# Optimization experiments

Measured on AMD Instinct MI355X. Metric: run time of the kernel, lower is better.

## Reference

```python
import jax, jax.numpy as jnp
import numpy as np

B, S = 4, 2048          # batch, seq tokens
D_IN, D_HID = 1280, 2048  # from CAMERAMOE emb_size / d_inner
E, K = 8, 2             # num_experts, top_k
LN_EPS = 1e-6


def setup_inputs() -> dict:
    key = jax.random.key(0)
    ks = jax.random.split(key, 8)
    rn = lambda k, shp, sc=1.0: jax.random.normal(k, shp, dtype=jnp.float32) * sc
    return {
        "x": rn(ks[0], (B, S, D_IN)),
        "noise": rn(ks[1], (B, S, E)),          # the randn_like draw, made explicit
        "wr": rn(ks[2], (D_IN, E), 0.02), "br": jnp.zeros((E,), jnp.float32),
        "wn": rn(ks[3], (D_IN, E), 0.02), "bn": jnp.zeros((E,), jnp.float32),
        "w1": rn(ks[4], (E, D_IN, D_HID), 0.02), "b1": jnp.zeros((E, D_HID), jnp.float32),
        "w2": rn(ks[5], (E, D_HID, D_IN), 0.02), "b2": jnp.zeros((E, D_IN), jnp.float32),
        "gamma": jnp.ones((E, D_IN), jnp.float32), "beta": jnp.zeros((E, D_IN), jnp.float32),
    }


def reference(x, noise, wr, br, wn, bn, w1, b1, w2, b2, gamma, beta):
    # --- NoisyTopkRouter ---
    logits = x @ wr + br                                  # [B,S,E]
    noise_logits = x @ wn + bn                            # [B,S,E]
    noisy = logits + noise * jax.nn.softplus(noise_logits)
    _, idx = jax.lax.top_k(noisy, K)                      # [B,S,K]
    sel = jax.nn.one_hot(idx, E, dtype=bool).any(axis=-2) # [B,S,E] selected-expert mask
    sparse_logits = jnp.where(sel, noisy, -jnp.inf)       # scatter of top-k logits into -inf
    gates = jax.nn.softmax(sparse_logits, axis=-1)        # zeros for non-selected experts

    # --- SparseMoE combine (gate-weighted sum over experts; gate==0 masks out
    # non-selected tokens, matching the torch masked gather/scatter-add math) ---
    h = jax.nn.relu(jnp.einsum('bsd,edh->ebsh', x, w1) + b1[:, None, None, :])
    y = jnp.einsum('ebsh,ehd->ebsd', h, w2) + b2[:, None, None, :]
    y = y + x                                             # residual (broadcast over E)
    mu = y.mean(axis=-1, keepdims=True)
    var = y.var(axis=-1, keepdims=True)
    y = (y - mu) * jax.lax.rsqrt(var + LN_EPS)
    y = y * gamma[:, None, None, :] + beta[:, None, None, :]
    return jnp.einsum('ebsd,bse->bsd', y, gates)          # [B,S,D_IN]
```

## Files before the change

### kernel.cpp

```cpp
#include <hip/hip_runtime.h>
#include <stdint.h>

typedef unsigned short u16;
typedef __attribute__((ext_vector_type(8))) short short8;
typedef __attribute__((ext_vector_type(4))) float f32x4;
typedef __attribute__((ext_vector_type(4))) float float4v;
typedef __attribute__((ext_vector_type(4))) unsigned short us4;
typedef __attribute__((ext_vector_type(8))) unsigned short us8;

#define TOK   8192
#define DIN   1280
#define DHID  2048
#define NEXP  8
#define RCAP  17408
#define MT128 136

#define TRBLK1 5120
#define TRBLK2 5120

__device__ __forceinline__ float bf2f(u16 u) {
  union { unsigned int i; float f; } v; v.i = ((unsigned int)u) << 16; return v.f;
}
__device__ __forceinline__ u16 f2bf(float f) {
  union { float f; unsigned int i; } v; v.f = f;
  unsigned int x = v.i;
  return (u16)((x + 0x7fffu + ((x >> 16) & 1u)) >> 16);
}

__device__ __forceinline__ void gload16(const u16* g, void* lds) {
  __builtin_amdgcn_global_load_lds(
      (const __attribute__((address_space(1))) unsigned int*)g,
      (__attribute__((address_space(3))) unsigned int*)lds, 16, 0, 0);
}

__global__ __launch_bounds__(256) void tr_k(
    const float* __restrict__ w1, u16* __restrict__ W1t,
    const float* __restrict__ w2, u16* __restrict__ W2t)
{
  __shared__ u16 ldsT[64 * 72];
  int id = blockIdx.x;
  int tid = threadIdx.x;
  int w = tid >> 6, lane = tid & 63;

  const float* in; u16* outp; int RK, CN, rb, cb;
  if (id < TRBLK1) {
    int e = id / 640, r = id % 640;
    RK = DIN; CN = DHID;
    rb = (r >> 5) * 64; cb = (r & 31) * 64;
    in = w1 + (size_t)e * RK * CN; outp = W1t + (size_t)e * RK * CN;
  } else {
    int id2 = id - TRBLK1;
    int e = id2 / 640, r = id2 % 640;
    RK = DHID; CN = DIN;
    rb = (r / 20) * 64; cb = (r % 20) * 64;
    in = w2 + (size_t)e * RK * CN; outp = W2t + (size_t)e * RK * CN;
  }
  {
    const float* src = in + (size_t)(rb + lane) * CN + cb + w * 16;
    u16 val[16];
    #pragma unroll
    for (int k = 0; k < 4; k++) {
      float4v v = *(const float4v*)(src + k * 4);
      #pragma unroll
      for (int j = 0; j < 4; j++) val[k * 4 + j] = f2bf(v[j]);
    }
    #pragma unroll
    for (int j = 0; j < 16; j++)
      ldsT[(w * 16 + j) * 72 + lane] = val[j];
  }
  __syncthreads();
  {
    int oc = tid >> 2, rch = (tid & 3) * 16;
    const u16* s = &ldsT[oc * 72 + rch];
    u16* d = outp + (size_t)(cb + oc) * RK + rb + rch;
    *(us8*)(d)     = *(const us8*)(s);
    *(us8*)(d + 8) = *(const us8*)(s + 8);
  }
}

__global__ __launch_bounds__(256) void router_k(
    const float* __restrict__ x, const float* __restrict__ noise,
    const float* __restrict__ wr, const float* __restrict__ br,
    const float* __restrict__ wn, const float* __restrict__ bn,
    int* __restrict__ topk_e, float* __restrict__ topk_g)
{
  int w = threadIdx.x >> 6, lane = threadIdx.x & 63;
  int t0 = blockIdx.x * 8 + w * 2;
  int h = lane & 1, dl = lane >> 1;
  const float* xA = x + (size_t)t0 * DIN;
  const float* xB = xA + DIN;

  float ra[4], na[4], rb2[4], nb2[4];
  #pragma unroll
  for (int j = 0; j < 4; j++) { ra[j] = 0.f; na[j] = 0.f; rb2[j] = 0.f; nb2[j] = 0.f; }

  #pragma unroll 4
  for (int d0 = 0; d0 < DIN; d0 += 32) {
    int d = d0 + dl;
    float4v wrv = *(const float4v*)(wr + (size_t)d * 8 + h * 4);
    float4v wnv = *(const float4v*)(wn + (size_t)d * 8 + h * 4);
    float xa = xA[d], xb = xB[d];
    #pragma unroll
    for (int j = 0; j < 4; j++) {
      ra[j]  += xa * wrv[j]; na[j]  += xa * wnv[j];
      rb2[j] += xb * wrv[j]; nb2[j] += xb * wnv[j];
    }
  }
  #pragma unroll
  for (int off = 2; off < 64; off <<= 1) {
    #pragma unroll
    for (int j = 0; j < 4; j++) {
      ra[j]  += __shfl_xor(ra[j],  off);
      na[j]  += __shfl_xor(na[j],  off);
      rb2[j] += __shfl_xor(rb2[j], off);
      nb2[j] += __shfl_xor(nb2[j], off);
    }
  }
  float raO[4], naO[4], rbO[4], nbO[4];
  #pragma unroll
  for (int j = 0; j < 4; j++) {
    raO[j] = __shfl_xor(ra[j], 1);
    naO[j] = __shfl_xor(na[j], 1);
    rbO[j] = __shfl_xor(rb2[j], 1);
    nbO[j] = __shfl_xor(nb2[j], 1);
  }
  if (lane == 0) {
    #pragma unroll
    for (int tt = 0; tt < 2; tt++) {
      int t = t0 + tt;
      float noisy[8];
      #pragma unroll
      for (int j = 0; j < 4; j++) {
        float lg0 = (tt ? rb2[j] : ra[j]) + br[j];
        float nl0 = (tt ? nb2[j] : na[j]) + bn[j];
        float lg1 = (tt ? rbO[j] : raO[j]) + br[4 + j];
        float nl1 = (tt ? nbO[j] : naO[j]) + bn[4 + j];
        float sp0 = (nl0 > 0.f) ? nl0 + log1pf(expf(-nl0)) : log1pf(expf(nl0));
        float sp1 = (nl1 > 0.f) ? nl1 + log1pf(expf(-nl1)) : log1pf(expf(nl1));
        noisy[j]     = lg0 + noise[(size_t)t * 8 + j] * sp0;
        noisy[4 + j] = lg1 + noise[(size_t)t * 8 + 4 + j] * sp1;
      }
      int e0 = 0; float v0 = noisy[0];
      #pragma unroll
      for (int e = 1; e < 8; e++) if (noisy[e] > v0) { v0 = noisy[e]; e0 = e; }
      int e1 = -1; float v1 = -1e30f;
      #pragma unroll
      for (int e = 0; e < 8; e++) if (e != e0 && noisy[e] > v1) { v1 = noisy[e]; e1 = e; }
      float g0 = 1.f / (1.f + expf(v1 - v0));
      topk_e[2*t] = e0; topk_e[2*t+1] = e1;
      topk_g[2*t] = g0; topk_g[2*t+1] = 1.f - g0;
    }
  }
}

__global__ __launch_bounds__(1024) void scan_k(
    const int* __restrict__ topk_e, int* __restrict__ rowmap, int* __restrict__ aoffs)
{
  __shared__ int cnt[1024][8];
  __shared__ int tot[8];
  __shared__ int base[8];
  int tid = threadIdx.x;
  int ebuf[16];
  #pragma unroll
  for (int j = 0; j < 16; j++) ebuf[j] = topk_e[tid * 16 + j];
  int c0=0,c1=0,c2=0,c3=0,c4=0,c5=0,c6=0,c7=0;
  #pragma unroll
  for (int j = 0; j < 16; j++) {
    int e = ebuf[j];
    c0 += (e==0); c1 += (e==1); c2 += (e==2); c3 += (e==3);
    c4 += (e==4); c5 += (e==5); c6 += (e==6); c7 += (e==7);
  }
  cnt[tid][0]=c0; cnt[tid][1]=c1; cnt[tid][2]=c2; cnt[tid][3]=c3;
  cnt[tid][4]=c4; cnt[tid][5]=c5; cnt[tid][6]=c6; cnt[tid][7]=c7;
  __syncthreads();

  int w = tid >> 6, lane = tid & 63;
  if (w < 8) {
    int e = w;
    int s[16]; int run = 0;
    #pragma unroll
    for (int j = 0; j < 16; j++) { s[j] = run; run += cnt[lane*16+j][e]; }
    int inc = run;
    for (int off = 1; off < 64; off <<= 1) {
      int v = __shfl_up(inc, off);
      if (lane >= off) inc += v;
    }
    int lane_excl = inc - run;
    #pragma unroll
    for (int j = 0; j < 16; j++) cnt[lane*16+j][e] = lane_excl + s[j];
    if (lane == 63) tot[e] = inc;
  }
  __syncthreads();
  if (tid == 0) {
    int a = 0;
    for (int e = 0; e < 8; e++) { base[e] = a; aoffs[e] = a; a += (tot[e] + 127) & ~127; }
    aoffs[8] = a;
  }
  __syncthreads();
  int o0 = base[0]+cnt[tid][0], o1 = base[1]+cnt[tid][1], o2 = base[2]+cnt[tid][2],
      o3 = base[3]+cnt[tid][3], o4 = base[4]+cnt[tid][4], o5 = base[5]+cnt[tid][5],
      o6 = base[6]+cnt[tid][6], o7 = base[7]+cnt[tid][7];
  #pragma unroll
  for (int j = 0; j < 16; j++) {
    int e = ebuf[j];
    int row = o0;
    row = (e==1) ? o1 : row; row = (e==2) ? o2 : row; row = (e==3) ? o3 : row;
    row = (e==4) ? o4 : row; row = (e==5) ? o5 : row; row = (e==6) ? o6 : row;
    row = (e==7) ? o7 : row;
    o0 += (e==0); o1 += (e==1); o2 += (e==2); o3 += (e==3);
    o4 += (e==4); o5 += (e==5); o6 += (e==6); o7 += (e==7);
    rowmap[tid * 16 + j] = row;
  }
}

__global__ __launch_bounds__(256) void gather_k(
    const float* __restrict__ x, const int* __restrict__ rowmap,
    u16* __restrict__ Xe)
{
  int w = threadIdx.x >> 6, lane = threadIdx.x & 63;
  int t = blockIdx.x * 4 + w;
  int r0 = rowmap[2*t], r1 = rowmap[2*t+1];
  const float4v* xs = (const float4v*)(x + (size_t)t * DIN);
  us4* d0 = (us4*)(Xe + (size_t)r0 * DIN);
  us4* d1 = (us4*)(Xe + (size_t)r1 * DIN);
  #pragma unroll
  for (int i = 0; i < DIN / 4 / 64; i++) {
    int q = i * 64 + lane;
    float4v v = xs[q];
    us4 o;
    #pragma unroll
    for (int j = 0; j < 4; j++) o[j] = f2bf(v[j]);
    d0[q] = o;
    d1[q] = o;
  }
}

__global__ __launch_bounds__(256, 2) void gemm128_k(
    const u16* __restrict__ A, const u16* __restrict__ Bt,
    const float* __restrict__ bias, u16* __restrict__ Out,
    const int* __restrict__ aoffs, int K, int N, int relu)
{
  extern __shared__ u16 sm[];

  int nwgx = gridDim.x;
  int id = blockIdx.y * nwgx + blockIdx.x;
  int per = (nwgx * gridDim.y) >> 3;
  int sid = (id & 7) * per + (id >> 3);
  int bx = sid % nwgx, by = sid / nwgx;

  int row0 = by * 128;
  if (row0 >= aoffs[NEXP]) return;
  int e = 0;
  #pragma unroll
  for (int i = 0; i < NEXP; i++) if (row0 >= aoffs[i + 1]) e = i + 1;
  int ncol0 = bx * 128;
  const u16* Ab = A + (size_t)row0 * K;
  const u16* Bb = Bt + ((size_t)e * N + ncol0) * K;

  int tid = threadIdx.x, w = tid >> 6, lane = tid & 63;
  int wr = w >> 1, wc = w & 1;
  int l15 = lane & 15, l4 = lane >> 4;
  int xorv = (l15 & 7) << 3;

  int srow[4], skc[4];
  #pragma unroll
  for (int q = 0; q < 4; q++) {
    int cd = q * 256 + tid;
    int cs = cd ^ ((cd >> 3) & 7);
    srow[q] = cs >> 3;
    skc[q]  = (cs & 7) * 8;
  }
  int ldsw = w * 1024;

  f32x4 acc[4][4];
  #pragma unroll
  for (int m = 0; m < 4; m++)
    #pragma unroll
    for (int n = 0; n < 4; n++) acc[m][n] = (f32x4){0.f, 0.f, 0.f, 0.f};

  short8 a[4][2], b0[2][2], b1[2][2];

#define STAGE_A(T, BUF) do {                                                  \
    char* d_ = (char*)sm + (BUF) * 32768;                                     \
    int ko_ = (T) * 64;                                                       \
    _Pragma("unroll")                                                         \
    for (int q = 0; q < 4; q++)                                               \
      gload16(Ab + (size_t)srow[q] * K + ko_ + skc[q], d_ + q*4096 + ldsw);   \
  } while (0)
#define STAGE_B(T, BUF) do {                                                  \
    char* d_ = (char*)sm + (BUF) * 32768 + 16384;                             \
    int ko_ = (T) * 64;                                                       \
    _Pragma("unroll")                                                         \
    for (int q = 0; q < 4; q++)                                               \
      gload16(Bb + (size_t)srow[q] * K + ko_ + skc[q], d_ + q*4096 + ldsw);   \
  } while (0)
#define RD_A() do {                                                           \
    _Pragma("unroll")                                                         \
    for (int m = 0; m < 4; m++)                                               \
      _Pragma("unroll")                                                       \
      for (int ks = 0; ks < 2; ks++) {                                        \
        int r_ = wr*64 + m*16 + l15;                                          \
        a[m][ks] = *(const short8*)&smA[(r_*64 + ks*32 + l4*8) ^ xorv];       \
      }                                                                       \
  } while (0)
#define RD_B(DST, NH) do {                                                    \
    _Pragma("unroll")                                                         \
    for (int n = 0; n < 2; n++)                                               \
      _Pragma("unroll")                                                       \
      for (int ks = 0; ks < 2; ks++) {                                        \
        int r_ = wc*64 + (NH)*32 + n*16 + l15;                                \
        DST[n][ks] = *(const short8*)&smB[(r_*64 + ks*32 + l4*8) ^ xorv];     \
      }                                                                       \
  } while (0)
#define MFMA16(NH, BB) do {                                                   \
    _Pragma("unroll")                                                         \
    for (int m = 0; m < 4; m++)                                               \
      _Pragma("unroll")                                                       \
      for (int n = 0; n < 2; n++)                                             \
        _Pragma("unroll")                                                     \
        for (int ks = 0; ks < 2; ks++)                                        \
          acc[m][(NH)*2+n] = __builtin_amdgcn_mfma_f32_16x16x32_bf16(         \
              a[m][ks], BB[n][ks], acc[m][(NH)*2+n], 0, 0, 0);                \
  } while (0)
#define BAR __builtin_amdgcn_s_barrier()

  int NT = K >> 6;
  STAGE_A(0, 0);
  STAGE_B(0, 0);
  STAGE_A(1, 1);
  STAGE_B(1, 1);
  asm volatile("s_waitcnt vmcnt(8)" ::: "memory");
  BAR;

  for (int t = 0; t < NT; ++t) {
    int buf = t & 1;
    const u16* smA = sm + buf * 16384;
    const u16* smB = smA + 8192;
    RD_A();
    RD_B(b0, 0);
    RD_B(b1, 1);
    asm volatile("s_waitcnt lgkmcnt(0)" ::: "memory");
    BAR;
    if (t + 2 < NT) {
      STAGE_A(t + 2, buf);
      STAGE_B(t + 2, buf);
    }
    __builtin_amdgcn_s_setprio(1);
    MFMA16(0, b0);
    MFMA16(1, b1);
    __builtin_amdgcn_s_setprio(0);
    if (t + 2 < NT) {
      asm volatile("s_waitcnt vmcnt(8)" ::: "memory");
    } else if (t + 1 < NT) {
      asm volatile("s_waitcnt vmcnt(0)" ::: "memory");
    }
    BAR;
  }
#undef STAGE_A
#undef STAGE_B
#undef RD_A
#undef RD_B
#undef MFMA16
#undef BAR

  #pragma unroll
  for (int in = 0; in < 4; in++) {
    int c = ncol0 + wc * 64 + in * 16 + l15;
    float bv = bias[(size_t)e * N + c];
    #pragma unroll
    for (int im = 0; im < 4; im++) {
      int rb = row0 + wr * 64 + im * 16 + l4 * 4;
      #pragma unroll
      for (int j = 0; j < 4; j++) {
        float v = acc[im][in][j] + bv;
        if (relu) v = fmaxf(v, 0.f);
        Out[(size_t)(rb + j) * N + c] = f2bf(v);
      }
    }
  }
}

__global__ __launch_bounds__(256) void ln_k(
    const float* __restrict__ x, const u16* __restrict__ Y,
    const int* __restrict__ rowmap, const int* __restrict__ topk_e,
    const float* __restrict__ topk_g, const float* __restrict__ gamma,
    const float* __restrict__ beta, float* __restrict__ out)
{
  __shared__ float red[4][4];
  int t = blockIdx.x, tid = threadIdx.x;
  int r0 = rowmap[2*t], r1 = rowmap[2*t+1];
  int e0 = topk_e[2*t], e1 = topk_e[2*t+1];
  float g0 = topk_g[2*t], g1 = topk_g[2*t+1];
  const float* xt = x + (size_t)t * DIN;
  const u16* y0p = Y + (size_t)r0 * DIN;
  const u16* y1p = Y + (size_t)r1 * DIN;
  float v0[5], v1[5];
  float s0 = 0.f, q0 = 0.f, s1 = 0.f, q1 = 0.f;
  #pragma unroll
  for (int i = 0; i < 5; i++) {
    int d = i * 256 + tid;
    float xv = xt[d];
    float a = xv + bf2f(y0p[d]);
    float b = xv + bf2f(y1p[d]);
    v0[i] = a; v1[i] = b;
    s0 += a; q0 += a * a; s1 += b; q1 += b * b;
  }
  for (int off = 32; off; off >>= 1) {
    s0 += __shfl_xor(s0, off); q0 += __shfl_xor(q0, off);
    s1 += __shfl_xor(s1, off); q1 += __shfl_xor(q1, off);
  }
  int w = tid >> 6, lane = tid & 63;
  if (lane == 0) { red[w][0] = s0; red[w][1] = q0; red[w][2] = s1; red[w][3] = q1; }
  __syncthreads();
  s0 = red[0][0] + red[1][0] + red[2][0] + red[3][0];
  q0 = red[0][1] + red[1][1] + red[2][1] + red[3][1];
  s1 = red[0][2] + red[1][2] + red[2][2] + red[3][2];
  q1 = red[0][3] + red[1][3] + red[2][3] + red[3][3];
  const float inv = 1.f / DIN;
  float mu0 = s0 * inv, mu1 = s1 * inv;
  float rs0 = rsqrtf(fmaxf(q0 * inv - mu0 * mu0, 0.f) + 1e-6f);
  float rs1 = rsqrtf(fmaxf(q1 * inv - mu1 * mu1, 0.f) + 1e-6f);
  const float* ga0 = gamma + (size_t)e0 * DIN;
  const float* be0 = beta  + (size_t)e0 * DIN;
  const float* ga1 = gamma + (size_t)e1 * DIN;
  const float* be1 = beta  + (size_t)e1 * DIN;
  #pragma unroll
  for (int i = 0; i < 5; i++) {
    int d = i * 256 + tid;
    float n0 = (v0[i] - mu0) * rs0 * ga0[d] + be0[d];
    float n1 = (v1[i] - mu1) * rs1 * ga1[d] + be1[d];
    out[(size_t)t * DIN + d] = g0 * n0 + g1 * n1;
  }
}

extern "C" void kernel_launch(void* const* d_in, const int* in_sizes, int n_in,
                              void* d_out, int out_size, void* d_ws, size_t ws_size,
                              hipStream_t stream)
{
  const float* x     = (const float*)d_in[0];
  const float* noise = (const float*)d_in[1];
  const float* wr    = (const float*)d_in[2];
  const float* br    = (const float*)d_in[3];
  const float* wn    = (const float*)d_in[4];
  const float* bn    = (const float*)d_in[5];
  const float* w1    = (const float*)d_in[6];
  const float* b1    = (const float*)d_in[7];
  const float* w2    = (const float*)d_in[8];
  const float* b2    = (const float*)d_in[9];
  const float* gamma = (const float*)d_in[10];
  const float* beta  = (const float*)d_in[11];
  float* out = (float*)d_out;
  char* ws = (char*)d_ws;

  int*   aoffs   = (int*)(ws + 128);
  int*   rowmap  = (int*)(ws + 4096);
  int*   topk_e  = (int*)(ws + 4096 + 65536);
  float* topk_g  = (float*)(ws + 4096 + 2 * 65536);

  const size_t XE_OFF   = (size_t)1 << 20;
  const size_t XE_BYTES = (size_t)RCAP * DIN * 2;
  const size_t H_BYTES  = (size_t)RCAP * DHID * 2;
  const size_t WT_BYTES = (size_t)NEXP * DHID * DIN * 2;
  u16* Xe  = (u16*)(ws + XE_OFF);
  u16* Hb  = (u16*)(ws + XE_OFF + XE_BYTES);
  u16* Yb  = Xe;
  u16* W1t = (u16*)(ws + XE_OFF + XE_BYTES + H_BYTES);
  u16* W2t = (u16*)(ws + XE_OFF + XE_BYTES + H_BYTES + WT_BYTES);

  router_k<<<TOK/8, 256, 0, stream>>>(x, noise, wr, br, wn, bn, topk_e, topk_g);
  scan_k<<<1, 1024, 0, stream>>>(topk_e, rowmap, aoffs);
  tr_k<<<TRBLK1 + TRBLK2, 256, 0, stream>>>(w1, W1t, w2, W2t);
  gather_k<<<TOK/4, 256, 0, stream>>>(x, rowmap, Xe);
  gemm128_k<<<dim3(DHID/128, MT128), 256, 65536, stream>>>(Xe, W1t, b1, Hb, aoffs, DIN, DHID, 1);
  gemm128_k<<<dim3(DIN/128, MT128), 256, 65536, stream>>>(Hb, W2t, b2, Yb, aoffs, DHID, DIN, 0);
  ln_k<<<TOK, 256, 0, stream>>>(x, Yb, rowmap, topk_e, topk_g, gamma, beta, out);
}
```

Before: 341.5 us.

## Merge transpose and gather kernels, halve GEMM K-tile, vectorize LayerNorm combine

Fuses the weight transpose/convert kernel with the token gather into one launch to drop a kernel boundary. The grouped GEMM moves from a 64-wide to a 32-wide K tile, which halves shared memory to 32KB and raises the occupancy hint from 2 to 4 blocks per CU. It also changes the LDS swizzle and drops the split B-fragment loads. The LayerNorm/combine kernel now handles one token per wavefront with float4 loads and no block-level reduction. The risks are more barriers per K step in the GEMM and register pressure under the tighter launch bound.

```diff
diff --git a/kernel.cpp b/kernel.cpp
--- a/kernel.cpp
+++ b/kernel.cpp
@@ -17,6 +17,7 @@
 
 #define TRBLK1 5120
 #define TRBLK2 5120
+#define GABLKS 2048
 
 __device__ __forceinline__ float bf2f(u16 u) {
   union { unsigned int i; float f; } v; v.i = ((unsigned int)u) << 16; return v.f;
@@ -31,51 +32,6 @@
   __builtin_amdgcn_global_load_lds(
       (const __attribute__((address_space(1))) unsigned int*)g,
       (__attribute__((address_space(3))) unsigned int*)lds, 16, 0, 0);
-}
-
-__global__ __launch_bounds__(256) void tr_k(
-    const float* __restrict__ w1, u16* __restrict__ W1t,
-    const float* __restrict__ w2, u16* __restrict__ W2t)
-{
-  __shared__ u16 ldsT[64 * 72];
-  int id = blockIdx.x;
-  int tid = threadIdx.x;
-  int w = tid >> 6, lane = tid & 63;
-
-  const float* in; u16* outp; int RK, CN, rb, cb;
-  if (id < TRBLK1) {
-    int e = id / 640, r = id % 640;
-    RK = DIN; CN = DHID;
-    rb = (r >> 5) * 64; cb = (r & 31) * 64;
-    in = w1 + (size_t)e * RK * CN; outp = W1t + (size_t)e * RK * CN;
-  } else {
-    int id2 = id - TRBLK1;
-    int e = id2 / 640, r = id2 % 640;
-    RK = DHID; CN = DIN;
-    rb = (r / 20) * 64; cb = (r % 20) * 64;
-    in = w2 + (size_t)e * RK * CN; outp = W2t + (size_t)e * RK * CN;
-  }
-  {
-    const float* src = in + (size_t)(rb + lane) * CN + cb + w * 16;
-    u16 val[16];
-    #pragma unroll
-    for (int k = 0; k < 4; k++) {
-      float4v v = *(const float4v*)(src + k * 4);
-      #pragma unroll
-      for (int j = 0; j < 4; j++) val[k * 4 + j] = f2bf(v[j]);
-    }
-    #pragma unroll
-    for (int j = 0; j < 16; j++)
-      ldsT[(w * 16 + j) * 72 + lane] = val[j];
-  }
-  __syncthreads();
-  {
-    int oc = tid >> 2, rch = (tid & 3) * 16;
-    const u16* s = &ldsT[oc * 72 + rch];
-    u16* d = outp + (size_t)(cb + oc) * RK + rb + rch;
-    *(us8*)(d)     = *(const us8*)(s);
-    *(us8*)(d + 8) = *(const us8*)(s + 8);
-  }
 }
 
 __global__ __launch_bounds__(256) void router_k(
@@ -213,12 +169,56 @@
   }
 }
 
-__global__ __launch_bounds__(256) void gather_k(
+__global__ __launch_bounds__(256) void trga_k(
+    const float* __restrict__ w1, u16* __restrict__ W1t,
+    const float* __restrict__ w2, u16* __restrict__ W2t,
     const float* __restrict__ x, const int* __restrict__ rowmap,
     u16* __restrict__ Xe)
 {
-  int w = threadIdx.x >> 6, lane = threadIdx.x & 63;
-  int t = blockIdx.x * 4 + w;
+  __shared__ u16 ldsT[64 * 72];
+  int id = blockIdx.x;
+  int tid = threadIdx.x;
+  int w = tid >> 6, lane = tid & 63;
+
+  if (id < TRBLK1 + TRBLK2) {
+    const float* in; u16* outp; int RK, CN, rb, cb;
+    if (id < TRBLK1) {
+      int e = id / 640, r = id % 640;
+      RK = DIN; CN = DHID;
+      rb = (r >> 5) * 64; cb = (r & 31) * 64;
+      in = w1 + (size_t)e * RK * CN; outp = W1t + (size_t)e * RK * CN;
+    } else {
+      int id2 = id - TRBLK1;
+      int e = id2 / 640, r = id2 % 640;
+      RK = DHID; CN = DIN;
+      rb = (r / 20) * 64; cb = (r % 20) * 64;
+      in = w2 + (size_t)e * RK * CN; outp = W2t + (size_t)e * RK * CN;
+    }
+    {
+      const float* src = in + (size_t)(rb + lane) * CN + cb + w * 16;
+      u16 val[16];
+      #pragma unroll
+      for (int k = 0; k < 4; k++) {
+        float4v v = *(const float4v*)(src + k * 4);
+        #pragma unroll
+        for (int j = 0; j < 4; j++) val[k * 4 + j] = f2bf(v[j]);
+      }
+      #pragma unroll
+      for (int j = 0; j < 16; j++)
+        ldsT[(w * 16 + j) * 72 + lane] = val[j];
+    }
+    __syncthreads();
+    {
+      int oc = tid >> 2, rch = (tid & 3) * 16;
+      const u16* s = &ldsT[oc * 72 + rch];
+      u16* d = outp + (size_t)(cb + oc) * RK + rb + rch;
+      *(us8*)(d)     = *(const us8*)(s);
+      *(us8*)(d + 8) = *(const us8*)(s + 8);
+    }
+    return;
+  }
+
+  int t = (id - (TRBLK1 + TRBLK2)) * 4 + w;
   int r0 = rowmap[2*t], r1 = rowmap[2*t+1];
   const float4v* xs = (const float4v*)(x + (size_t)t * DIN);
   us4* d0 = (us4*)(Xe + (size_t)r0 * DIN);
@@ -235,7 +235,7 @@
   }
 }
 
-__global__ __launch_bounds__(256, 2) void gemm128_k(
+__global__ __launch_bounds__(256, 4) void gemm128_k(
     const u16* __restrict__ A, const u16* __restrict__ Bt,
     const float* __restrict__ bias, u16* __restrict__ Out,
     const int* __restrict__ aoffs, int K, int N, int relu)
@@ -260,15 +260,15 @@
   int tid = threadIdx.x, w = tid >> 6, lane = tid & 63;
   int wr = w >> 1, wc = w & 1;
   int l15 = lane & 15, l4 = lane >> 4;
-  int xorv = (l15 & 7) << 3;
-
-  int srow[4], skc[4];
-  #pragma unroll
-  for (int q = 0; q < 4; q++) {
+  int xsw = (l15 >> 1) & 3;
+
+  int srow[2], skc[2];
+  #pragma unroll
+  for (int q = 0; q < 2; q++) {
     int cd = q * 256 + tid;
-    int cs = cd ^ ((cd >> 3) & 7);
-    srow[q] = cs >> 3;
-    skc[q]  = (cs & 7) * 8;
+    int cs = cd ^ ((cd >> 3) & 3);
+    srow[q] = cs >> 2;
+    skc[q]  = (cs & 3) * 8;
   }
   int ldsw = w * 1024;
 
@@ -278,67 +278,60 @@
     #pragma unroll
     for (int n = 0; n < 4; n++) acc[m][n] = (f32x4){0.f, 0.f, 0.f, 0.f};
 
-  short8 a[4][2], b0[2][2], b1[2][2];
+  short8 a[4], b[4];
 
 #define STAGE_A(T, BUF) do {                                                  \
-    char* d_ = (char*)sm + (BUF) * 32768;                                     \
-    int ko_ = (T) * 64;                                                       \
+    char* d_ = (char*)sm + (BUF) * 16384;                                     \
+    int ko_ = (T) * 32;                                                       \
     _Pragma("unroll")                                                         \
-    for (int q = 0; q < 4; q++)                                               \
+    for (int q = 0; q < 2; q++)                                               \
       gload16(Ab + (size_t)srow[q] * K + ko_ + skc[q], d_ + q*4096 + ldsw);   \
   } while (0)
 #define STAGE_B(T, BUF) do {                                                  \
-    char* d_ = (char*)sm + (BUF) * 32768 + 16384;                             \
-    int ko_ = (T) * 64;                                                       \
+    char* d_ = (char*)sm + (BUF) * 16384 + 8192;                              \
+    int ko_ = (T) * 32;                                                       \
     _Pragma("unroll")                                                         \
-    for (int q = 0; q < 4; q++)                                               \
+    for (int q = 0; q < 2; q++)                                               \
       gload16(Bb + (size_t)srow[q] * K + ko_ + skc[q], d_ + q*4096 + ldsw);   \
   } while (0)
 #define RD_A() do {                                                           \
     _Pragma("unroll")                                                         \
-    for (int m = 0; m < 4; m++)                                               \
-      _Pragma("unroll")                                                       \
-      for (int ks = 0; ks < 2; ks++) {                                        \
-        int r_ = wr*64 + m*16 + l15;                                          \
-        a[m][ks] = *(const short8*)&smA[(r_*64 + ks*32 + l4*8) ^ xorv];       \
-      }                                                                       \
+    for (int m = 0; m < 4; m++) {                                             \
+      int r_ = wr*64 + m*16 + l15;                                            \
+      a[m] = *(const short8*)&smA[r_*32 + ((l4 ^ xsw) * 8)];                  \
+    }                                                                         \
   } while (0)
-#define RD_B(DST, NH) do {                                                    \
+#define RD_B() do {                                                           \
     _Pragma("unroll")                                                         \
-    for (int n = 0; n < 2; n++)                                               \
-      _Pragma("unroll")                                                       \
-      for (int ks = 0; ks < 2; ks++) {                                        \
-        int r_ = wc*64 + (NH)*32 + n*16 + l15;                                \
-        DST[n][ks] = *(const short8*)&smB[(r_*64 + ks*32 + l4*8) ^ xorv];     \
-      }                                                                       \
+    for (int n = 0; n < 4; n++) {                                             \
+      int r_ = wc*64 + n*16 + l15;                                            \
+      b[n] = *(const short8*)&smB[r_*32 + ((l4 ^ xsw) * 8)];                  \
+    }                                                                         \
   } while (0)
-#define MFMA16(NH, BB) do {                                                   \
+#define MFMA16() do {                                                         \
     _Pragma("unroll")                                                         \
     for (int m = 0; m < 4; m++)                                               \
       _Pragma("unroll")                                                       \
-      for (int n = 0; n < 2; n++)                                             \
-        _Pragma("unroll")                                                     \
-        for (int ks = 0; ks < 2; ks++)                                        \
-          acc[m][(NH)*2+n] = __builtin_amdgcn_mfma_f32_16x16x32_bf16(         \
-              a[m][ks], BB[n][ks], acc[m][(NH)*2+n], 0, 0, 0);                \
+      for (int n = 0; n < 4; n++)                                             \
+        acc[m][n] = __builtin_amdgcn_mfma_f32_16x16x32_bf16(                  \
+            a[m], b[n], acc[m][n], 0, 0, 0);                                  \
   } while (0)
 #define BAR __builtin_amdgcn_s_barrier()
 
-  int NT = K >> 6;
+  int NT = K >> 5;
   STAGE_A(0, 0);
   STAGE_B(0, 0);
   STAGE_A(1, 1);
   STAGE_B(1, 1);
-  asm volatile("s_waitcnt vmcnt(8)" ::: "memory");
+  asm volatile("s_waitcnt vmcnt(4)" ::: "memory");
   BAR;
 
   for (int t = 0; t < NT; ++t) {
     int buf = t & 1;
-    const u16* smA = sm + buf * 16384;
-    const u16* smB = smA + 8192;
+    const u16* smA = sm + buf * 8192;
+    const u16* smB = smA + 4096;
     RD_A();
-    RD_B(b0, 0);
-    RD_B(b1, 1);
+    RD_B();
     asm volatile("s_waitcnt lgkmcnt(0)" ::: "memory");
     BAR;
     if (t + 2 < NT) {
@@ -346,11 +339,10 @@
       STAGE_B(t + 2, buf);
     }
     __builtin_amdgcn_s_setprio(1);
-    MFMA16(0, b0);
-    MFMA16(1, b1);
+    MFMA16();
     __builtin_amdgcn_s_setprio(0);
     if (t + 2 < NT) {
-      asm volatile("s_waitcnt vmcnt(8)" ::: "memory");
+      asm volatile("s_waitcnt vmcnt(4)" ::: "memory");
     } else if (t + 1 < NT) {
       asm volatile("s_waitcnt vmcnt(0)" ::: "memory");
     }
@@ -386,50 +378,55 @@
     const float* __restrict__ topk_g, const float* __restrict__ gamma,
     const float* __restrict__ beta, float* __restrict__ out)
 {
-  __shared__ float red[4][4];
-  int t = blockIdx.x, tid = threadIdx.x;
+  int w = threadIdx.x >> 6, lane = threadIdx.x & 63;
+  int t = blockIdx.x * 4 + w;
   int r0 = rowmap[2*t], r1 = rowmap[2*t+1];
   int e0 = topk_e[2*t], e1 = topk_e[2*t+1];
   float g0 = topk_g[2*t], g1 = topk_g[2*t+1];
-  const float* xt = x + (size_t)t * DIN;
-  const u16* y0p = Y + (size_t)r0 * DIN;
-  const u16* y1p = Y + (size_t)r1 * DIN;
-  float v0[5], v1[5];
+  const float4v* xt = (const float4v*)(x + (size_t)t * DIN);
+  const us4* y0p = (const us4*)(Y + (size_t)r0 * DIN);
+  const us4* y1p = (const us4*)(Y + (size_t)r1 * DIN);
+  float4v v0[5], v1[5];
   float s0 = 0.f, q0 = 0.f, s1 = 0.f, q1 = 0.f;
   #pragma unroll
   for (int i = 0; i < 5; i++) {
-    int d = i * 256 + tid;
-    float xv = xt[d];
-    float a = xv + bf2f(y0p[d]);
-    float b = xv + bf2f(y1p[d]);
-    v0[i] = a; v1[i] = b;
-    s0 += a; q0 += a * a; s1 += b; q1 += b * b;
-  }
+    int q = i * 64 + lane;
+    float4v xv = xt[q];
+    us4 ya = y0p[q], yb = y1p[q];
+    #pragma unroll
+    for (int j = 0; j < 4; j++) {
+      float aa = xv[j] + bf2f(ya[j]);
+      float bb = xv[j] + bf2f(yb[j]);
+      v0[i][j] = aa; v1[i][j] = bb;
+      s0 += aa; q0 += aa * aa; s1 += bb; q1 += bb * bb;
+    }
+  }
+  #pragma unroll
   for (int off = 32; off; off >>= 1) {
     s0 += __shfl_xor(s0, off); q0 += __shfl_xor(q0, off);
     s1 += __shfl_xor(s1, off); q1 += __shfl_xor(q1, off);
   }
-  int w = tid >> 6, lane = tid & 63;
-  if (lane == 0) { red[w][0] = s0; red[w][1] = q0; red[w][2] = s1; red[w][3] = q1; }
-  __syncthreads();
-  s0 = red[0][0] + red[1][0] + red[2][0] + red[3][0];
-  q0 = red[0][1] + red[1][1] + red[2][1] + red[3][1];
-  s1 = red[0][2] + red[1][2] + red[2][2] + red[3][2];
-  q1 = red[0][3] + red[1][3] + red[2][3] + red[3][3];
   const float inv = 1.f / DIN;
   float mu0 = s0 * inv, mu1 = s1 * inv;
   float rs0 = rsqrtf(fmaxf(q0 * inv - mu0 * mu0, 0.f) + 1e-6f);
   float rs1 = rsqrtf(fmaxf(q1 * inv - mu1 * mu1, 0.f) + 1e-6f);
-  const float* ga0 = gamma + (size_t)e0 * DIN;
-  const float* be0 = beta  + (size_t)e0 * DIN;
-  const float* ga1 = gamma + (size_t)e1 * DIN;
-  const float* be1 = beta  + (size_t)e1 * DIN;
+  const float4v* ga0 = (const float4v*)(gamma + (size_t)e0 * DIN);
+  const float4v* be0 = (const float4v*)(beta  + (size_t)e0 * DIN);
+  const float4v* ga1 = (const float4v*)(gamma + (size_t)e1 * DIN);
+  const float4v* be1 = (const float4v*)(beta  + (size_t)e1 * DIN);
+  float4v* op = (float4v*)(out + (size_t)t * DIN);
   #pragma unroll
   for (int i = 0; i < 5; i++) {
-    int d = i * 256 + tid;
-    float n0 = (v0[i] - mu0) * rs0 * ga0[d] + be0[d];
-    float n1 = (v1[i] - mu1) * rs1 * ga1[d] + be1[d];
-    out[(size_t)t * DIN + d] = g0 * n0 + g1 * n1;
+    int q = i * 64 + lane;
+    float4v gA = ga0[q], bA = be0[q], gB = ga1[q], bB = be1[q];
+    float4v o;
+    #pragma unroll
+    for (int j = 0; j < 4; j++) {
+      float n0 = (v0[i][j] - mu0) * rs0 * gA[j] + bA[j];
+      float n1 = (v1[i][j] - mu1) * rs1 * gB[j] + bB[j];
+      o[j] = g0 * n0 + g1 * n1;
+    }
+    op[q] = o;
   }
 }
 
@@ -469,9 +466,8 @@
 
   router_k<<<TOK/8, 256, 0, stream>>>(x, noise, wr, br, wn, bn, topk_e, topk_g);
   scan_k<<<1, 1024, 0, stream>>>(topk_e, rowmap, aoffs);
-  tr_k<<<TRBLK1 + TRBLK2, 256, 0, stream>>>(w1, W1t, w2, W2t);
-  gather_k<<<TOK/4, 256, 0, stream>>>(x, rowmap, Xe);
-  gemm128_k<<<dim3(DHID/128, MT128), 256, 65536, stream>>>(Xe, W1t, b1, Hb, aoffs, DIN, DHID, 1);
-  gemm128_k<<<dim3(DIN/128, MT128), 256, 65536, stream>>>(Hb, W2t, b2, Yb, aoffs, DHID, DIN, 0);
-  ln_k<<<TOK, 256, 0, stream>>>(x, Yb, rowmap, topk_e, topk_g, gamma, beta, out);
-}
+  trga_k<<<TRBLK1 + TRBLK2 + GABLKS, 256, 0, stream>>>(w1, W1t, w2, W2t, x, rowmap, Xe);
+  gemm128_k<<<dim3(DHID/128, MT128), 256, 32768, stream>>>(Xe, W1t, b1, Hb, aoffs, DIN, DHID, 1);
+  gemm128_k<<<dim3(DIN/128, MT128), 256, 32768, stream>>>(Hb, W2t, b2, Yb, aoffs, DHID, DIN, 0);
+  ln_k<<<TOK/4, 256, 0, stream>>>(x, Yb, rowmap, topk_e, topk_g, gamma, beta, out);
+}
```

Measured after the change: 376.4 us. 10.2% more time.
